# Performance work log

Hardware: AMD Instinct MI355X
Metric: run time of the kernel (lower is better)

Reference implementation:

```python
import jax, jax.numpy as jnp
import numpy as np

KSIZE = 7
NSPIX = 196


def _unfold(x, k):
    # x: (T, C, H, W) -> (T, C, k*k, H, W), reflect padding, torch Unfold ordering
    p = (k - 1) // 2
    T, C, H, W = x.shape
    xp = jnp.pad(x, ((0, 0), (0, 0), (p, p), (p, p)), mode='reflect')
    return jnp.stack([xp[:, :, i:i + H, j:j + W] for i in range(k) for j in range(k)], axis=2)


def setup_inputs() -> dict:
    key = jax.random.key(0)
    k1, k2, k3, k4, k5 = jax.random.split(key, 5)
    T, C, H, W = 2, 64, 160, 160
    fan_in = C * KSIZE * KSIZE
    x = jax.random.normal(k1, (T, C, H, W), jnp.float32)
    spix = jax.random.randint(k2, (T, H, W), 0, NSPIX, jnp.int32)
    W_lin = jax.random.normal(k3, (C, fan_in), jnp.float32) / np.sqrt(fan_in)
    b_lin = jax.random.normal(k4, (C,), jnp.float32) * 0.01
    w_scale = jax.random.normal(k5, (C,), jnp.float32) / np.sqrt(C)
    b_scale = jnp.zeros((1,), jnp.float32)
    return {"x": x, "spix": spix, "W_lin": W_lin, "b_lin": b_lin,
            "w_scale": w_scale, "b_scale": b_scale}


def reference(x, spix, W_lin, b_lin, w_scale, b_scale):
    T, C, H, W = x.shape
    K2 = KSIZE * KSIZE
    O = W_lin.shape[0]
    p = (KSIZE - 1) // 2

    # unfold(x) with reflect padding -> patches (T, C, K2, H, W)
    patches = _unfold(x, KSIZE)

    # unfold(spix) -> neighbor superpixel ids per pixel (T, K2, H, W)
    sp = jnp.pad(spix, ((0, 0), (p, p), (p, p)), mode='reflect')
    nb = jnp.stack([sp[:, i:i + H, j:j + W] for i in range(KSIZE) for j in range(KSIZE)], axis=1)

    # per-frame superpixel mean pooling (bist.get_pooled_video): down (T, S, C)
    seg = (spix.astype(jnp.int32) + jnp.arange(T, dtype=jnp.int32)[:, None, None] * NSPIX).reshape(-1)
    feats = x.transpose(0, 2, 3, 1).reshape(-1, C)  # (T*H*W, C)
    sums = jax.ops.segment_sum(feats, seg, num_segments=T * NSPIX).reshape(T, NSPIX, C)
    cnts = jax.ops.segment_sum(jnp.ones((seg.shape[0],), x.dtype), seg,
                               num_segments=T * NSPIX).reshape(T, NSPIX, 1)
    down = sums / jnp.maximum(cnts, 1.0)

    # squared pairwise distances between superpixel means: pwd (T, S, S)
    sq = jnp.sum(down * down, axis=-1)
    pwd = jnp.maximum(sq[:, :, None] + sq[:, None, :]
                      - 2.0 * jnp.einsum('tsc,tuc->tsu', down, down), 0.0)

    # sims[t,k,h,w] = ||mean(spix[t,h,w]) - mean(nb[t,k,h,w])||^2
    tidx = jnp.arange(T)[:, None, None, None]
    sims = pwd[tidx, spix[:, None, :, :], nb]  # (T, K2, H, W)

    # scale = 10 * softplus(1x1-conv(x / ||x||_c))  -> (T, H, W)
    xn = x / (jnp.linalg.norm(x, axis=1, keepdims=True) + 1e-10)
    scale = 10.0 * jax.nn.softplus(jnp.einsum('c,tchw->thw', w_scale, xn) + b_scale[0])

    # apply_norm 'exp_max' over the kernel-tap axis
    rw = jnp.exp(-scale[:, None, :, :] * sims)  # (T, K2, H, W)
    rw = rw / (1e-5 + jnp.max(rw, axis=1, keepdims=True))

    # dynamic conv: out[t,o,h,w] = sum_{c,k} W[o,c,k] * patches[t,c,k,h,w] * rw[t,k,h,w] + b[o]
    out = jnp.einsum('ock,tckhw,tkhw->tohw', W_lin.reshape(O, C, K2), patches, rw)
    return out + b_lin[None, :, None, None]
```

## Files before the change

kernel.cpp:

```cpp
#include <hip/hip_runtime.h>
#include <math.h>

#define TT 2
#define CC 64
#define HH 160
#define WW 160
#define KS 7
#define K2 49
#define NSPIX 196
#define HWSZ (HH*WW)
#define PAD 3
#define OO 64
#define FANIN (CC*K2)
#define TS 8
#define PS (TS+KS-1)
#define NPOS (PS*PS)

#define NCHUNK 25
#define CHUNKPIX 1024

typedef _Float16 half8 __attribute__((ext_vector_type(8)));
typedef float f32x16 __attribute__((ext_vector_type(16)));
typedef unsigned int uint4v __attribute__((ext_vector_type(4)));
typedef _Float16 half2v __attribute__((ext_vector_type(2)));

__device__ __forceinline__ int reflect(int i, int n) {
    if (i < 0) i = -i;
    if (i >= n) i = 2*n - 2 - i;
    return i;
}

__global__ __launch_bounds__(256) void k_prep(const float* __restrict__ x,
                                              const int* __restrict__ spix,
                                              const float* __restrict__ Wl,
                                              const float* __restrict__ wsc,
                                              const float* __restrict__ bsc,
                                              float* __restrict__ sums,
                                              float* __restrict__ cnts,
                                              float* __restrict__ scale,
                                              _Float16* __restrict__ Wb,
                                              _Float16* __restrict__ xT) {
    __shared__ float ls[8*200];
    __shared__ float lcnt[200];
    int bid = blockIdx.x;
    int tid = threadIdx.x;

    if (bid < 400) {
        int cg = bid & 7;
        int rest = bid >> 3;
        int ch = rest % NCHUNK;
        int t  = rest / NCHUNK;

        for (int i = tid; i < 8*200; i += 256) ls[i] = 0.f;
        if (cg == 0) for (int i = tid; i < 200; i += 256) lcnt[i] = 0.f;
        __syncthreads();

        int base = ch*CHUNKPIX;
        const float* xb = x + ((size_t)t*CC + cg*8)*HWSZ;
        #pragma unroll
        for (int i = 0; i < CHUNKPIX; i += 256) {
            int pix = base + i + tid;
            int s = spix[t*HWSZ + pix];
            if (cg == 0) atomicAdd(&lcnt[s], 1.0f);
            #pragma unroll
            for (int j = 0; j < 8; ++j) atomicAdd(&ls[j*200 + s], xb[(size_t)j*HWSZ + pix]);
        }
        __syncthreads();

        float* sb = sums + (size_t)t*NSPIX*CC + cg*8;
        for (int i = tid; i < 8*NSPIX; i += 256) {
            int s = i >> 3, j = i & 7;
            float v = ls[j*200 + s];
            if (v != 0.f) atomicAdd(&sb[s*CC + j], v);
        }
        if (cg == 0)
            for (int i = tid; i < NSPIX; i += 256) {
                float v = lcnt[i];
                if (v != 0.f) atomicAdd(&cnts[t*NSPIX + i], v);
            }
    } else if (bid < 600) {
        int pix = (bid - 400)*256 + tid;
        int t = pix / HWSZ, hw = pix - t*HWSZ;
        const float* xs = x + (size_t)t*CC*HWSZ + hw;
        float s1 = 0.f, s2 = 0.f;
        unsigned int pk[32];
        #pragma unroll
        for (int cp = 0; cp < 32; ++cp) {
            float v0 = xs[(size_t)(2*cp)*HWSZ];
            float v1 = xs[(size_t)(2*cp + 1)*HWSZ];
            s1 += wsc[2*cp]*v0 + wsc[2*cp+1]*v1;
            s2 = fmaf(v0, v0, s2); s2 = fmaf(v1, v1, s2);
            half2v h; h[0] = (_Float16)v0; h[1] = (_Float16)v1;
            pk[cp] = __builtin_bit_cast(unsigned int, h);
        }
        float z = s1/(sqrtf(s2) + 1e-10f) + bsc[0];
        float sp_ = (z > 0.f) ? z + log1pf(expf(-z)) : log1pf(expf(z));
        scale[pix] = 10.f*sp_;
        uint4v* dst = (uint4v*)(xT + (size_t)pix*64);
        #pragma unroll
        for (int q = 0; q < 8; ++q) {
            uint4v v = { pk[4*q], pk[4*q+1], pk[4*q+2], pk[4*q+3] };
            dst[q] = v;
        }
    } else {
        int row = (bid - 600)*256 + tid;
        if (row < 2*K2*4*64) {
            int ln  = row & 63;
            int kc  = (row >> 6) & 3;
            int tq  = row >> 8;
            int tap = tq % K2;
            int qo  = tq / K2;
            int o = qo*32 + (ln & 31);
            int cb = kc*16 + (ln >> 5)*8;
            _Float16* dst = Wb + (size_t)row*8;
            const float* src = Wl + (size_t)o*FANIN + tap;
            #pragma unroll
            for (int j = 0; j < 8; ++j) dst[j] = (_Float16)src[(size_t)(cb + j)*K2];
        }
    }
}

__global__ __launch_bounds__(256) void k_pwd(const float* __restrict__ sums,
                                             const float* __restrict__ cnts,
                                             float* __restrict__ pwd) {
    int tid = blockIdx.x*256 + threadIdx.x;
    if (tid >= TT*NSPIX*NSPIX) return;
    int t = tid / (NSPIX*NSPIX); int r = tid - t*NSPIX*NSPIX;
    int s = r / NSPIX, u = r - (r / NSPIX)*NSPIX;
    const float* ds = sums + (size_t)(t*NSPIX + s)*CC;
    const float* du = sums + (size_t)(t*NSPIX + u)*CC;
    float is = 1.0f / fmaxf(cnts[t*NSPIX + s], 1.0f);
    float iu = 1.0f / fmaxf(cnts[t*NSPIX + u], 1.0f);
    float acc = 0.f;
    #pragma unroll 8
    for (int c = 0; c < CC; ++c) {
        float d = ds[c]*is - du[c]*iu;
        acc = fmaf(d, d, acc);
    }
    pwd[tid] = acc;
}

__global__ __launch_bounds__(256, 4) void k_main(
    const _Float16* __restrict__ xT, const int* __restrict__ spix,
    const _Float16* __restrict__ Wb, const float* __restrict__ b_lin,
    const float* __restrict__ pwd, const float* __restrict__ scale,
    float* __restrict__ out)
{
    __shared__ unsigned short xpT[NPOS*64];
    __shared__ unsigned int   rwb[K2*64];
    __shared__ int   sp[NPOS];
    __shared__ float mxp[4*64];

    int bid = blockIdx.x;
    int t = bid / 400;
    int r = bid - t*400;
    int th0 = (r / 20)*TS, tw0 = (r - (r/20)*20)*TS;
    int tid = threadIdx.y*64 + threadIdx.x;

    for (int i = tid; i < NPOS; i += 256) {
        int rr = reflect(th0 + i/PS - PAD, HH);
        int cc = reflect(tw0 + i%PS - PAD, WW);
        sp[i] = spix[t*HWSZ + rr*WW + cc];
    }
    {
        const _Float16* xt = xT + (size_t)t*HWSZ*64;
        for (int i = tid; i < NPOS*8; i += 256) {
            int pos = i >> 3, cb = i & 7;
            int rr = reflect(th0 + pos/PS - PAD, HH);
            int cc = reflect(tw0 + pos%PS - PAD, WW);
            uint4v v = *(const uint4v*)(xt + (size_t)(rr*WW + cc)*64 + cb*8);
            int chunk = cb ^ (pos & 7);
            *(uint4v*)&xpT[pos*64 + chunk*8] = v;
        }
    }
    __syncthreads();

    int p_ = threadIdx.x;
    int ty = threadIdx.y;
    int py0 = p_ >> 3, px0 = p_ & 7;
    {
        float sc = scale[t*HWSZ + (th0 + py0)*WW + (tw0 + px0)];
        int s0 = sp[(py0 + PAD)*PS + (px0 + PAD)];
        const float* pr = pwd + (t*NSPIX + s0)*NSPIX;
        float pmax = 0.f;
        for (int k = ty; k < K2; k += 4) {
            int di = k/KS, dj = k - di*KS;
            int nb = sp[(py0 + di)*PS + (px0 + dj)];
            float v = __expf(-sc * pr[nb]);
            _Float16 h = (_Float16)v;
            half2v hp; hp[0] = h; hp[1] = h;
            rwb[k*64 + p_] = __builtin_bit_cast(unsigned int, hp);
            pmax = fmaxf(pmax, v);
        }
        mxp[ty*64 + p_] = pmax;
    }
    __syncthreads();

    int ln = threadIdx.x;
    int wv = __builtin_amdgcn_readfirstlane(threadIdx.y);
    int qp = wv & 1, kh = wv >> 1;
    int p  = qp*32 + (ln & 31);
    int ppy = p >> 3, ppx = p & 7;
    int lhi = ln >> 5;

    int jc0 = 4*kh + lhi, jc1 = jc0 + 2;

    const _Float16* a0p = Wb + (size_t)(2*kh)*512 + ln*8;
    const _Float16* a1p = a0p + (size_t)K2*4*512;

    f32x16 acc0, acc1;
    #pragma unroll
    for (int i = 0; i < 16; ++i) { acc0[i] = 0.f; acc1[i] = 0.f; }

    half8 A00 = *(const half8*)(a0p);
    half8 A01 = *(const half8*)(a0p + 512);
    half8 A10 = *(const half8*)(a1p);
    half8 A11 = *(const half8*)(a1p + 512);
    int pos0 = ppy*PS + ppx;
    int sw0  = pos0 & 7;
    const unsigned short* bb0 = &xpT[pos0*64];
    half8 B0 = *(const half8*)(bb0 + ((jc0 ^ sw0) << 3));
    half8 B1 = *(const half8*)(bb0 + ((jc1 ^ sw0) << 3));
    unsigned int rv = rwb[p];

    int di = 0, dj = 0;
    #pragma unroll 8
    for (int tap = 0; tap < K2 - 1; ++tap) {
        if (++dj == KS) { dj = 0; ++di; }
        a0p += 2048; a1p += 2048;
        half8 nA00 = *(const half8*)(a0p);
        half8 nA01 = *(const half8*)(a0p + 512);
        half8 nA10 = *(const half8*)(a1p);
        half8 nA11 = *(const half8*)(a1p + 512);
        int npos = (ppy + di)*PS + (ppx + dj);
        int nsw  = npos & 7;
        const unsigned short* nbb = &xpT[npos*64];
        half8 nB0 = *(const half8*)(nbb + ((jc0 ^ nsw) << 3));
        half8 nB1 = *(const half8*)(nbb + ((jc1 ^ nsw) << 3));
        unsigned int nrv = rwb[(tap + 1)*64 + p];

        half2v rh = __builtin_bit_cast(half2v, rv);
        half8 rv8 = { rh[0], rh[1], rh[0], rh[1], rh[0], rh[1], rh[0], rh[1] };
        half8 b0 = B0 * rv8;
        half8 b1 = B1 * rv8;
        acc0 = __builtin_amdgcn_mfma_f32_32x32x16_f16(A00, b0, acc0, 0, 0, 0);
        acc1 = __builtin_amdgcn_mfma_f32_32x32x16_f16(A10, b0, acc1, 0, 0, 0);
        acc0 = __builtin_amdgcn_mfma_f32_32x32x16_f16(A01, b1, acc0, 0, 0, 0);
        acc1 = __builtin_amdgcn_mfma_f32_32x32x16_f16(A11, b1, acc1, 0, 0, 0);

        A00 = nA00; A01 = nA01; A10 = nA10; A11 = nA11;
        B0 = nB0; B1 = nB1; rv = nrv;
    }
    {
        half2v rh = __builtin_bit_cast(half2v, rv);
        half8 rv8 = { rh[0], rh[1], rh[0], rh[1], rh[0], rh[1], rh[0], rh[1] };
        half8 b0 = B0 * rv8;
        half8 b1 = B1 * rv8;
        acc0 = __builtin_amdgcn_mfma_f32_32x32x16_f16(A00, b0, acc0, 0, 0, 0);
        acc1 = __builtin_amdgcn_mfma_f32_32x32x16_f16(A10, b0, acc1, 0, 0, 0);
        acc0 = __builtin_amdgcn_mfma_f32_32x32x16_f16(A01, b1, acc0, 0, 0, 0);
        acc1 = __builtin_amdgcn_mfma_f32_32x32x16_f16(A11, b1, acc1, 0, 0, 0);
    }

    __syncthreads();
    float* red = (float*)xpT;
    if (kh == 1) {
        #pragma unroll
        for (int i = 0; i < 16; ++i) {
            red[((qp*2 + 0)*16 + i)*64 + ln] = acc0[i];
            red[((qp*2 + 1)*16 + i)*64 + ln] = acc1[i];
        }
    }
    __syncthreads();
    if (kh == 0) {
        float m = fmaxf(fmaxf(mxp[p], mxp[64 + p]), fmaxf(mxp[128 + p], mxp[192 + p]));
        float s = 1.f/(1e-5f + m);
        int h = th0 + ppy, w = tw0 + ppx;
        int row_hi = 4*lhi;
        float* ob = out + (size_t)t*OO*HWSZ + h*WW + w;
        #pragma unroll
        for (int rg = 0; rg < 16; ++rg) {
            int o0 = (rg & 3) + 8*(rg >> 2) + row_hi;
            int o1 = 32 + o0;
            float v0 = acc0[rg] + red[((qp*2 + 0)*16 + rg)*64 + ln];
            float v1 = acc1[rg] + red[((qp*2 + 1)*16 + rg)*64 + ln];
            ob[(size_t)o0*HWSZ] = v0*s + b_lin[o0];
            ob[(size_t)o1*HWSZ] = v1*s + b_lin[o1];
        }
    }
}

extern "C" void kernel_launch(void* const* d_in, const int* in_sizes, int n_in,
                              void* d_out, int out_size, void* d_ws, size_t ws_size,
                              hipStream_t stream) {
    const float* x    = (const float*)d_in[0];
    const int*   spix = (const int*)d_in[1];
    const float* Wl   = (const float*)d_in[2];
    const float* bl   = (const float*)d_in[3];
    const float* wsc  = (const float*)d_in[4];
    const float* bsc  = (const float*)d_in[5];
    float* out = (float*)d_out;

    float* ws    = (float*)d_ws;
    float* sums  = ws;
    float* cnts  = sums + TT*NSPIX*CC;
    float* pwd   = cnts + TT*NSPIX;
    float* scale = pwd  + TT*NSPIX*NSPIX;
    _Float16* Wb = (_Float16*)(scale + TT*HWSZ);
    _Float16* xT = Wb + (size_t)2*K2*4*64*8;

    hipMemsetAsync(sums, 0, (size_t)(TT*NSPIX*CC + TT*NSPIX)*sizeof(float), stream);

    k_prep<<<698, 256, 0, stream>>>(x, spix, Wl, wsc, bsc, sums, cnts, scale, Wb, xT);
    k_pwd <<<(TT*NSPIX*NSPIX + 255)/256, 256, 0, stream>>>(sums, cnts, pwd);

    dim3 blk(64, 4, 1);
    k_main<<<TT*400, blk, 0, stream>>>(xT, spix, Wb, bl, pwd, scale, out);
}
```

Baseline: 150.4 us.

## Stage weight tiles into LDS via async global_load_lds double buffering

Weight fragments for each tap are no longer loaded straight from global memory into registers. They are staged into a double-buffered LDS array with global_load_lds, and the next tap's tile is prefetched while the current one feeds the MFMAs. The reweight buffer shrinks to 16-bit entries, and launch bounds drop from 4 to 3 blocks per SM to make room for the extra LDS. This adds a block-wide barrier every tap and removes the register-level software pipelining. The stageA call has no explicit wait for the async load, so correctness depends on the barrier draining it.

After: 174.8 us. 1.16x slower.

```diff
diff --git a/kernel.cpp b/kernel.cpp
--- a/kernel.cpp
+++ b/kernel.cpp
@@ -140,14 +140,27 @@
     pwd[tid] = acc;
 }
 
-__global__ __launch_bounds__(256, 4) void k_main(
+__device__ __forceinline__ void stageA(const _Float16* __restrict__ Wb,
+                                       _Float16* dstbuf, int tap, int w, int ln) {
+    const _Float16* g0 = Wb + (size_t)tap*2048 + (w*64 + ln)*8;
+    const _Float16* g1 = g0 + (size_t)K2*2048;
+    _Float16* l0 = dstbuf + w*512;
+    _Float16* l1 = dstbuf + 2048 + w*512;
+    __builtin_amdgcn_global_load_lds((const __attribute__((address_space(1))) unsigned int*)g0,
+                                     (__attribute__((address_space(3))) unsigned int*)l0, 16, 0, 0);
+    __builtin_amdgcn_global_load_lds((const __attribute__((address_space(1))) unsigned int*)g1,
+                                     (__attribute__((address_space(3))) unsigned int*)l1, 16, 0, 0);
+}
+
+__global__ __launch_bounds__(256, 3) void k_main(
     const _Float16* __restrict__ xT, const int* __restrict__ spix,
     const _Float16* __restrict__ Wb, const float* __restrict__ b_lin,
     const float* __restrict__ pwd, const float* __restrict__ scale,
     float* __restrict__ out)
 {
     __shared__ unsigned short xpT[NPOS*64];
-    __shared__ unsigned int   rwb[K2*64];
+    __shared__ unsigned short rwb[K2*64];
+    __shared__ _Float16 Ast[2][4096];
     __shared__ int   sp[NPOS];
     __shared__ float mxp[4*64];
 
@@ -174,6 +187,9 @@
         }
     }
     __syncthreads();
+
+    int ln = threadIdx.x;
+    int wv = __builtin_amdgcn_readfirstlane(threadIdx.y);
 
     int p_ = threadIdx.x;
     int ty = threadIdx.y;
@@ -187,82 +203,58 @@
             int di = k/KS, dj = k - di*KS;
             int nb = sp[(py0 + di)*PS + (px0 + dj)];
             float v = __expf(-sc * pr[nb]);
-            _Float16 h = (_Float16)v;
-            half2v hp; hp[0] = h; hp[1] = h;
-            rwb[k*64 + p_] = __builtin_bit_cast(unsigned int, hp);
+            rwb[k*64 + p_] = __builtin_bit_cast(unsigned short, (_Float16)v);
             pmax = fmaxf(pmax, v);
         }
         mxp[ty*64 + p_] = pmax;
     }
+    stageA(Wb, &Ast[0][0], 0, wv, ln);
     __syncthreads();
 
-    int ln = threadIdx.x;
-    int wv = __builtin_amdgcn_readfirstlane(threadIdx.y);
     int qp = wv & 1, kh = wv >> 1;
     int p  = qp*32 + (ln & 31);
     int ppy = p >> 3, ppx = p & 7;
     int lhi = ln >> 5;
 
     int jc0 = 4*kh + lhi, jc1 = jc0 + 2;
-
-    const _Float16* a0p = Wb + (size_t)(2*kh)*512 + ln*8;
-    const _Float16* a1p = a0p + (size_t)K2*4*512;
+    int aoff = 2*kh*512 + ln*8;
 
     f32x16 acc0, acc1;
     #pragma unroll
     for (int i = 0; i < 16; ++i) { acc0[i] = 0.f; acc1[i] = 0.f; }
 
-    half8 A00 = *(const half8*)(a0p);
-    half8 A01 = *(const half8*)(a0p + 512);
-    half8 A10 = *(const half8*)(a1p);
-    half8 A11 = *(const half8*)(a1p + 512);
-    int pos0 = ppy*PS + ppx;
-    int sw0  = pos0 & 7;
-    const unsigned short* bb0 = &xpT[pos0*64];
-    half8 B0 = *(const half8*)(bb0 + ((jc0 ^ sw0) << 3));
-    half8 B1 = *(const half8*)(bb0 + ((jc1 ^ sw0) << 3));
-    unsigned int rv = rwb[p];
-
+    int buf = 0;
     int di = 0, dj = 0;
-    #pragma unroll 8
-    for (int tap = 0; tap < K2 - 1; ++tap) {
-        if (++dj == KS) { dj = 0; ++di; }
-        a0p += 2048; a1p += 2048;
-        half8 nA00 = *(const half8*)(a0p);
-        half8 nA01 = *(const half8*)(a0p + 512);
-        half8 nA10 = *(const half8*)(a1p);
-        half8 nA11 = *(const half8*)(a1p + 512);
-        int npos = (ppy + di)*PS + (ppx + dj);
-        int nsw  = npos & 7;
-        const unsigned short* nbb = &xpT[npos*64];
-        half8 nB0 = *(const half8*)(nbb + ((jc0 ^ nsw) << 3));
-        half8 nB1 = *(const half8*)(nbb + ((jc1 ^ nsw) << 3));
-        unsigned int nrv = rwb[(tap + 1)*64 + p];
-
-        half2v rh = __builtin_bit_cast(half2v, rv);
-        half8 rv8 = { rh[0], rh[1], rh[0], rh[1], rh[0], rh[1], rh[0], rh[1] };
+    for (int tap = 0; tap < K2; ++tap) {
+        if (tap + 1 < K2) stageA(Wb, &Ast[buf ^ 1][0], tap + 1, wv, ln);
+
+        const _Float16* ab = &Ast[buf][aoff];
+        half8 A00 = *(const half8*)(ab);
+        half8 A01 = *(const half8*)(ab + 512);
+        half8 A10 = *(const half8*)(ab + 2048);
+        half8 A11 = *(const half8*)(ab + 2048 + 512);
+
+        int pos = (ppy + di)*PS + (ppx + dj);
+        int sw  = pos & 7;
+        const unsigned short* bbase = &xpT[pos*64];
+        half8 B0 = *(const half8*)(bbase + ((jc0 ^ sw) << 3));
+        half8 B1 = *(const half8*)(bbase + ((jc1 ^ sw) << 3));
+
+        _Float16 rh = __builtin_bit_cast(_Float16, rwb[tap*64 + p]);
+        half8 rv8 = { rh, rh, rh, rh, rh, rh, rh, rh };
         half8 b0 = B0 * rv8;
         half8 b1 = B1 * rv8;
+
         acc0 = __builtin_amdgcn_mfma_f32_32x32x16_f16(A00, b0, acc0, 0, 0, 0);
         acc1 = __builtin_amdgcn_mfma_f32_32x32x16_f16(A10, b0, acc1, 0, 0, 0);
         acc0 = __builtin_amdgcn_mfma_f32_32x32x16_f16(A01, b1, acc0, 0, 0, 0);
         acc1 = __builtin_amdgcn_mfma_f32_32x32x16_f16(A11, b1, acc1, 0, 0, 0);
 
-        A00 = nA00; A01 = nA01; A10 = nA10; A11 = nA11;
-        B0 = nB0; B1 = nB1; rv = nrv;
-    }
-    {
-        half2v rh = __builtin_bit_cast(half2v, rv);
-        half8 rv8 = { rh[0], rh[1], rh[0], rh[1], rh[0], rh[1], rh[0], rh[1] };
-        half8 b0 = B0 * rv8;
-        half8 b1 = B1 * rv8;
-        acc0 = __builtin_amdgcn_mfma_f32_32x32x16_f16(A00, b0, acc0, 0, 0, 0);
-        acc1 = __builtin_amdgcn_mfma_f32_32x32x16_f16(A10, b0, acc1, 0, 0, 0);
-        acc0 = __builtin_amdgcn_mfma_f32_32x32x16_f16(A01, b1, acc0, 0, 0, 0);
-        acc1 = __builtin_amdgcn_mfma_f32_32x32x16_f16(A11, b1, acc1, 0, 0, 0);
-    }
-
-    __syncthreads();
+        if (++dj == KS) { dj = 0; ++di; }
+        __syncthreads();
+        buf ^= 1;
+    }
+
     float* red = (float*)xpT;
     if (kh == 1) {
         #pragma unroll
```
